# Kernel tuning notes

Hardware: AMD Instinct MI355X
Metric: run time of the kernel (lower is better)

Reference implementation:

```python
import jax, jax.numpy as jnp
import numpy as np

N = 50000   # nodes
E = 800000  # directed edges (self-loops added inside reference)
F_IN, H, C = 128, 96, 32


def setup_inputs() -> dict:
    key = jax.random.key(0)
    ks = jax.random.split(key, 8)
    x = jax.random.normal(ks[0], (N, F_IN), dtype=jnp.float32)
    edge_index = jax.random.randint(ks[1], (2, E), 0, N, dtype=jnp.int64)
    W1 = jax.random.normal(ks[2], (F_IN, H), dtype=jnp.float32) * 0.05
    b1 = jnp.zeros((H,), dtype=jnp.float32)
    W2 = jax.random.normal(ks[3], (H, H), dtype=jnp.float32) * 0.05
    b2 = jnp.zeros((H,), dtype=jnp.float32)
    W3 = jax.random.normal(ks[4], (H, C), dtype=jnp.float32) * 0.05
    b3 = jnp.zeros((C,), dtype=jnp.float32)
    return {"x": x, "edge_index": edge_index, "W1": W1, "b1": b1,
            "W2": W2, "b2": b2, "W3": W3, "b3": b3}


def gcn_conv(x, W, b, src, dst, n):
    """PyG GCNConv: x' = D^{-1/2} (A+I) D^{-1/2} (x W) + b (self-loops in src/dst)."""
    xw = x @ W                                        # [n, out]
    ones = jnp.ones(src.shape[0], dtype=xw.dtype)
    deg = jax.ops.segment_sum(ones, dst, num_segments=n)
    dinv = jnp.where(deg > 0, jax.lax.rsqrt(jnp.maximum(deg, 1.0)), 0.0)
    norm = dinv[src] * dinv[dst]                      # [E+n]
    msg = norm[:, None] * xw[src]                     # gather + scale
    out = jax.ops.segment_sum(msg, dst, num_segments=n)  # scatter-add
    return out + b


def reference(x, edge_index, W1, b1, W2, b2, W3, b3):
    loop = jnp.arange(N, dtype=edge_index.dtype)
    src = jnp.concatenate([edge_index[0], loop])      # add self-loops once
    dst = jnp.concatenate([edge_index[1], loop])
    h = jax.nn.relu(gcn_conv(x, W1, b1, src, dst, N))   # dropout is identity (eval)
    h = jax.nn.relu(gcn_conv(h, W2, b2, src, dst, N))
    h = gcn_conv(h, W3, b3, src, dst, N)
    return jax.nn.log_softmax(h, axis=1)
```

## Files before the change

### kernel.cpp

```cpp
#include <hip/hip_runtime.h>
#include <hip/hip_fp16.h>


typedef _Float16 half8 __attribute__((ext_vector_type(8)));
typedef float f32x4 __attribute__((ext_vector_type(4)));

constexpr int CAP = 64;
constexpr int NPB = 128;
constexpr int NBINS_P = 512;
constexpr int EPB = 4096;
constexpr int BCAP = 2560;

__device__ inline unsigned char f_to_fp8(float f) {
    f = fminf(fmaxf(f, -448.0f), 448.0f);
    unsigned short u = __half_as_ushort(__float2half(f * 0.00390625f));
    unsigned short mag = (unsigned short)((u & 0x7FFF) + 0x40);
    return (unsigned char)(((u >> 8) & 0x80) | (mag >> 7));
}

__device__ inline float2 fp8x2_to_f2_scaled(unsigned int w) {
    unsigned int lo = ((w << 7) & 0x3F80u) | ((w << 8) & 0x8000u);
    unsigned int hi = ((w >> 1) & 0x3F80u) | (w & 0x8000u);
    union { unsigned int u; __half2 h; } cv;
    cv.u = lo | (hi << 16);
    return __half22float2(cv.h);
}

__device__ inline float4 fp8x4_to_f4_scaled(unsigned int w) {
    float2 lo = fp8x2_to_f2_scaled(w & 0xFFFFu);
    float2 hi = fp8x2_to_f2_scaled(w >> 16);
    return {lo.x, lo.y, hi.x, hi.y};
}

__global__ __launch_bounds__(256) void prep_kernel(const int* __restrict__ ei, int twoE,
                                                   int* __restrict__ flags,
                                                   int* __restrict__ bin_cnt,
                                                   const float* __restrict__ W1,
                                                   const float* __restrict__ W2,
                                                   const float* __restrict__ W3,
                                                   __half* __restrict__ Wt1,
                                                   __half* __restrict__ Wt2,
                                                   __half* __restrict__ Wt3) {
    if (blockIdx.x == 0) {
        if (threadIdx.x < 8) flags[threadIdx.x] = 0;
        for (int b = threadIdx.x; b < NBINS_P; b += 256) bin_cnt[b] = 0;
        __syncthreads();
        int c = 0;
        for (int j = threadIdx.x; j < 2048 && j < twoE; j += 256) {
            if ((j & 1) && ei[j] != 0) c++;
        }
        if (c) atomicAdd(&flags[4], c);
        return;
    }
    int i = (blockIdx.x - 1) * 256 + threadIdx.x;
    if (i < 128 * 96) {
        int f = i / 128, k = i - f * 128;
        Wt1[i] = __float2half(W1[(size_t)k * 96 + f]);
    } else if (i < 128 * 96 + 96 * 96) {
        int j = i - 128 * 96;
        int f = j / 96, k = j - f * 96;
        Wt2[j] = __float2half(W2[(size_t)k * 96 + f]);
    } else if (i < 128 * 96 + 96 * 96 + 96 * 32) {
        int j = i - 128 * 96 - 96 * 96;
        int f = j / 96, k = j - f * 96;
        Wt3[j] = __float2half(W3[(size_t)k * 32 + f]);
    }
}

__device__ inline int ld_idx(const int* ei, int half_, int i, int E, bool i64) {
    return i64 ? ei[2 * (half_ * (size_t)E + i)] : ei[half_ * (size_t)E + i];
}

__global__ __launch_bounds__(256) void part_kernel(const int* __restrict__ ei,
                                                   const int* __restrict__ flags,
                                                   int* __restrict__ bin_cnt,
                                                   int* __restrict__ bins, int E, int n) {
    __shared__ int hist[NBINS_P], excl[NBINS_P], cur[NBINS_P], gpos[NBINS_P];
    __shared__ int tmp[256];
    __shared__ int stage[EPB];
    const int tid = threadIdx.x;
    const bool i64 = (flags[4] == 0);
    for (int b = tid; b < NBINS_P; b += 256) hist[b] = 0;
    __syncthreads();

    int v[EPB / 256];
    const int base = blockIdx.x * EPB;
#pragma unroll
    for (int j = 0; j < EPB / 256; j++) {
        int i = base + j * 256 + tid;
        v[j] = -1;
        if (i < E) {
            int s = ld_idx(ei, 0, i, E, i64);
            int d = ld_idx(ei, 1, i, E, i64);
            if ((unsigned)s < (unsigned)n && (unsigned)d < (unsigned)n) {
                int bin = d >> 7, ln = d & 127;
                v[j] = (bin << 23) | (ln << 16) | s;
                atomicAdd(&hist[bin], 1);
            }
        }
    }
    __syncthreads();
    int a0 = hist[2 * tid], a1 = hist[2 * tid + 1];
    int pairsum = a0 + a1;
    tmp[tid] = pairsum;
    __syncthreads();
    for (int off = 1; off < 256; off <<= 1) {
        int t = (tid >= off) ? tmp[tid - off] : 0;
        __syncthreads();
        tmp[tid] += t;
        __syncthreads();
    }
    int S = tmp[tid] - pairsum;
    excl[2 * tid] = S;
    excl[2 * tid + 1] = S + a0;
    cur[2 * tid] = S;
    cur[2 * tid + 1] = S + a0;
    __syncthreads();
    for (int b = tid; b < NBINS_P; b += 256)
        gpos[b] = hist[b] ? atomicAdd(&bin_cnt[b], hist[b]) : 0;
#pragma unroll
    for (int j = 0; j < EPB / 256; j++) {
        if (v[j] != -1) {
            int bin = ((unsigned)v[j]) >> 23;
            int p = atomicAdd(&cur[bin], 1);
            stage[p] = v[j];
        }
    }
    __syncthreads();
    int total = excl[NBINS_P - 1] + hist[NBINS_P - 1];
    for (int i = tid; i < total; i += 256) {
        int w = stage[i];
        int bin = ((unsigned)w) >> 23;
        int k = gpos[bin] + (i - excl[bin]);
        if (k < BCAP) bins[(size_t)bin * BCAP + k] = w;
    }
}

__global__ __launch_bounds__(256) void build_kernel(const int* __restrict__ bin_cnt,
                                                    const int* __restrict__ bins,
                                                    int* __restrict__ cnt,
                                                    unsigned short* __restrict__ csr, int n) {
    __shared__ unsigned short lcsr[NPB * CAP];
    __shared__ int lcnt[NPB];
    const int b = blockIdx.x, tid = threadIdx.x;
    for (int i = tid; i < NPB; i += 256) lcnt[i] = 0;
    __syncthreads();
    int m = min(bin_cnt[b], BCAP);
    for (int i = tid; i < m; i += 256) {
        int w = bins[(size_t)b * BCAP + i];
        int ln = (w >> 16) & 127;
        int p = atomicAdd(&lcnt[ln], 1);
        if (p < CAP) lcsr[ln * CAP + p] = (unsigned short)(w & 0xFFFF);
    }
    __syncthreads();
    const int node0 = b * NPB;
    const unsigned int* l32 = (const unsigned int*)lcsr;
    unsigned int* c32 = (unsigned int*)(csr + (size_t)node0 * CAP);
    for (int i = tid; i < NPB * CAP / 2; i += 256) {
        int node = node0 + (i >> 5);
        if (node < n) c32[i] = l32[i];
    }
    for (int t = tid; t < NPB; t += 256)
        if (node0 + t < n) cnt[node0 + t] = lcnt[t];
}

__device__ inline half8 to_h8(float4 u0, float4 u1) {
    half8 r;
    r[0] = (_Float16)u0.x; r[1] = (_Float16)u0.y; r[2] = (_Float16)u0.z; r[3] = (_Float16)u0.w;
    r[4] = (_Float16)u1.x; r[5] = (_Float16)u1.y; r[6] = (_Float16)u1.z; r[7] = (_Float16)u1.w;
    return r;
}

template <int K, int F, bool XF32, bool OUT8>
__global__ __launch_bounds__(256) void gemm_mfma(const void* __restrict__ X,
                                                 const __half* __restrict__ Wt,
                                                 const int* __restrict__ cnt,
                                                 void* __restrict__ out, int n) {
    constexpr int KP = K + 8;
    constexpr int FT = F / 16;
    constexpr int KC = K / 32;
    __shared__ _Float16 Wl[F * KP];
    for (int i = threadIdx.x; i < F * (K / 8); i += 256) {
        int f = i / (K / 8), c = i - f * (K / 8);
        *(half8*)&Wl[f * KP + c * 8] = *(const half8*)&Wt[(size_t)f * K + c * 8];
    }
    __syncthreads();
    const int wave = threadIdx.x >> 6, lane = threadIdx.x & 63;
    const int node0 = (blockIdx.x * 4 + wave) * 16;
    if (node0 >= n) return;
    const int m = lane & 15, q = lane >> 4;
    const int arow = min(node0 + m, n - 1);

    half8 af[KC];
    if (XF32) {
        const float* xp = (const float*)X + (size_t)arow * K + q * 8;
#pragma unroll
        for (int kc = 0; kc < KC; kc++) {
            float4 u0 = *(const float4*)(xp + kc * 32);
            float4 u1 = *(const float4*)(xp + kc * 32 + 4);
            af[kc] = to_h8(u0, u1);
        }
    } else {
        const __half* xp = (const __half*)X + (size_t)arow * K + q * 8;
#pragma unroll
        for (int kc = 0; kc < KC; kc++) af[kc] = *(const half8*)(xp + kc * 32);
    }

    f32x4 acc[FT];
#pragma unroll
    for (int t = 0; t < FT; t++) acc[t] = (f32x4)0.f;
#pragma unroll
    for (int kc = 0; kc < KC; kc++) {
#pragma unroll
        for (int t = 0; t < FT; t++) {
            half8 b = *(const half8*)&Wl[(t * 16 + m) * KP + kc * 32 + q * 8];
            acc[t] = __builtin_amdgcn_mfma_f32_16x16x32_f16(af[kc], b, acc[t], 0, 0, 0);
        }
    }
    float dv[4];
#pragma unroll
    for (int r = 0; r < 4; r++) {
        int node = node0 + q * 4 + r;
        dv[r] = (node < n) ? rsqrtf(1.0f + (float)cnt[node]) : 0.f;
    }
#pragma unroll
    for (int t = 0; t < FT; t++)
#pragma unroll
        for (int r = 0; r < 4; r++) {
            int node = node0 + q * 4 + r;
            if (node < n) {
                float vv = acc[t][r] * dv[r];
                if (OUT8)
                    ((unsigned char*)out)[(size_t)node * F + t * 16 + m] = f_to_fp8(vv);
                else
                    ((__half*)out)[(size_t)node * F + t * 16 + m] = __float2half(vv);
            }
        }
}

__global__ __launch_bounds__(256) void agg96_fp8(const unsigned char* __restrict__ xws,
                                                 const int* __restrict__ cnt,
                                                 const unsigned short* __restrict__ csr,
                                                 const float* __restrict__ bias,
                                                 __half* __restrict__ out, int n) {
    int node = blockIdx.x * 4 + (threadIdx.x >> 6);
    int lane = threadIdx.x & 63;
    if (node >= n) return;
    const int g = lane < 24 ? 0 : 1;
    const int c = g ? lane - 24 : lane;
    const bool act = lane < 48;
    int deg = cnt[node];
    int m = min(deg, CAP);
    float dvs = rsqrtf(1.0f + (float)deg) * 256.0f;
    const uint4* r4 = (const uint4*)(csr + (size_t)node * CAP);
    float4 a = {0.f, 0.f, 0.f, 0.f};
    if (lane < 24) {
        unsigned int w = *(const unsigned int*)(xws + (size_t)node * 96 + c * 4);
        a = fp8x4_to_f4_scaled(w);
    }
    int e = 0;
#define G96_U(pr_) (g ? ((pr_) >> 16) : ((pr_) & 0xFFFF))
#define G96_LD(u_) (*(const unsigned int*)(xws + (size_t)(u_) * 96 + c * 4))
    for (; e + 16 <= m; e += 16) {
        uint4 pa = r4[e >> 3], pb = r4[(e >> 3) + 1];
        if (act) {
            unsigned int w0 = G96_LD(G96_U(pa.x)), w1 = G96_LD(G96_U(pa.y));
            unsigned int w2 = G96_LD(G96_U(pa.z)), w3 = G96_LD(G96_U(pa.w));
            unsigned int w4 = G96_LD(G96_U(pb.x)), w5 = G96_LD(G96_U(pb.y));
            unsigned int w6 = G96_LD(G96_U(pb.z)), w7 = G96_LD(G96_U(pb.w));
            float4 f;
            f = fp8x4_to_f4_scaled(w0); a.x += f.x; a.y += f.y; a.z += f.z; a.w += f.w;
            f = fp8x4_to_f4_scaled(w1); a.x += f.x; a.y += f.y; a.z += f.z; a.w += f.w;
            f = fp8x4_to_f4_scaled(w2); a.x += f.x; a.y += f.y; a.z += f.z; a.w += f.w;
            f = fp8x4_to_f4_scaled(w3); a.x += f.x; a.y += f.y; a.z += f.z; a.w += f.w;
            f = fp8x4_to_f4_scaled(w4); a.x += f.x; a.y += f.y; a.z += f.z; a.w += f.w;
            f = fp8x4_to_f4_scaled(w5); a.x += f.x; a.y += f.y; a.z += f.z; a.w += f.w;
            f = fp8x4_to_f4_scaled(w6); a.x += f.x; a.y += f.y; a.z += f.z; a.w += f.w;
            f = fp8x4_to_f4_scaled(w7); a.x += f.x; a.y += f.y; a.z += f.z; a.w += f.w;
        }
    }
    if (e + 8 <= m) {
        uint4 pa = r4[e >> 3];
        if (act) {
            unsigned int w0 = G96_LD(G96_U(pa.x)), w1 = G96_LD(G96_U(pa.y));
            unsigned int w2 = G96_LD(G96_U(pa.z)), w3 = G96_LD(G96_U(pa.w));
            float4 f;
            f = fp8x4_to_f4_scaled(w0); a.x += f.x; a.y += f.y; a.z += f.z; a.w += f.w;
            f = fp8x4_to_f4_scaled(w1); a.x += f.x; a.y += f.y; a.z += f.z; a.w += f.w;
            f = fp8x4_to_f4_scaled(w2); a.x += f.x; a.y += f.y; a.z += f.z; a.w += f.w;
            f = fp8x4_to_f4_scaled(w3); a.x += f.x; a.y += f.y; a.z += f.z; a.w += f.w;
        }
        e += 8;
    }
    if (e + 4 <= m) {
        const unsigned int* r2 = (const unsigned int*)r4;
        unsigned int p0 = r2[e >> 1], p1 = r2[(e >> 1) + 1];
        if (act) {
            unsigned int w0 = G96_LD(G96_U(p0)), w1 = G96_LD(G96_U(p1));
            float4 f;
            f = fp8x4_to_f4_scaled(w0); a.x += f.x; a.y += f.y; a.z += f.z; a.w += f.w;
            f = fp8x4_to_f4_scaled(w1); a.x += f.x; a.y += f.y; a.z += f.z; a.w += f.w;
        }
        e += 4;
    }
    if (e + 2 <= m) {
        unsigned int p0 = ((const unsigned int*)r4)[e >> 1];
        if (act) {
            unsigned int w0 = G96_LD(G96_U(p0));
            float4 f = fp8x4_to_f4_scaled(w0);
            a.x += f.x; a.y += f.y; a.z += f.z; a.w += f.w;
        }
        e += 2;
    }
    if (e < m && lane < 24) {
        int u = ((const unsigned short*)r4)[e];
        float4 f = fp8x4_to_f4_scaled(G96_LD(u));
        a.x += f.x; a.y += f.y; a.z += f.z; a.w += f.w;
    }
#undef G96_U
#undef G96_LD
    float px = __shfl(a.x, lane + 24);
    float py = __shfl(a.y, lane + 24);
    float pz = __shfl(a.z, lane + 24);
    float pw = __shfl(a.w, lane + 24);
    if (lane < 24) {
        a.x += px; a.y += py; a.z += pz; a.w += pw;
        float4 bb = *(const float4*)&bias[c * 4];
        float r0 = fmaxf(fmaf(dvs, a.x, bb.x), 0.f);
        float r1 = fmaxf(fmaf(dvs, a.y, bb.y), 0.f);
        float r2 = fmaxf(fmaf(dvs, a.z, bb.z), 0.f);
        float r3 = fmaxf(fmaf(dvs, a.w, bb.w), 0.f);
        union { __half2 h[2]; uint2 u; } pk;
        pk.h[0] = __floats2half2_rn(r0, r1);
        pk.h[1] = __floats2half2_rn(r2, r3);
        *(uint2*)(out + (size_t)node * 96 + c * 4) = pk.u;
    }
}

__global__ __launch_bounds__(256) void agg32_lsm(const __half* __restrict__ xws,
                                                 const int* __restrict__ cnt,
                                                 const unsigned short* __restrict__ csr,
                                                 const float* __restrict__ bias,
                                                 float* __restrict__ out, int n) {
    int node = blockIdx.x * 4 + (threadIdx.x >> 6);
    int lane = threadIdx.x & 63;
    if (node >= n) return;
    const int g = lane >> 4, l = lane & 15;
    int deg = cnt[node];
    int m = min(deg, CAP);
    float dv = rsqrtf(1.0f + (float)deg);
    const uint4* r4 = (const uint4*)(csr + (size_t)node * CAP);
    float2 a = {0.f, 0.f};
    if (g == 0) a = __half22float2(*(const __half2*)(xws + (size_t)node * 32 + l * 2));
    auto ext = [](uint4 p, int j) -> int {
        unsigned int h = (j & 4) ? ((j & 2) ? p.w : p.z) : ((j & 2) ? p.y : p.x);
        return (j & 1) ? (int)(h >> 16) : (int)(h & 0xFFFF);
    };
    int e = 0;
    for (; e + 16 <= m; e += 16) {
        uint4 pa = r4[e >> 3], pb = r4[(e >> 3) + 1];
        int u0 = ext(pa, g), u1 = ext(pa, g + 4);
        int u2 = ext(pb, g), u3 = ext(pb, g + 4);
        float2 f0 = __half22float2(*(const __half2*)(xws + (size_t)u0 * 32 + l * 2));
        float2 f1 = __half22float2(*(const __half2*)(xws + (size_t)u1 * 32 + l * 2));
        float2 f2 = __half22float2(*(const __half2*)(xws + (size_t)u2 * 32 + l * 2));
        float2 f3 = __half22float2(*(const __half2*)(xws + (size_t)u3 * 32 + l * 2));
        a.x += f0.x + f1.x + f2.x + f3.x;
        a.y += f0.y + f1.y + f2.y + f3.y;
    }
    if (e + 8 <= m) {
        uint4 pa = r4[e >> 3];
        int u0 = ext(pa, g), u1 = ext(pa, g + 4);
        float2 f0 = __half22float2(*(const __half2*)(xws + (size_t)u0 * 32 + l * 2));
        float2 f1 = __half22float2(*(const __half2*)(xws + (size_t)u1 * 32 + l * 2));
        a.x += f0.x + f1.x;
        a.y += f0.y + f1.y;
        e += 8;
    }
    if (e + 4 <= m) {
        unsigned int p0 = ((const unsigned int*)r4)[e >> 1];
        unsigned int p1 = ((const unsigned int*)r4)[(e >> 1) + 1];
        unsigned int h = (g & 2) ? p1 : p0;
        int u = (g & 1) ? (int)(h >> 16) : (int)(h & 0xFFFF);
        float2 f = __half22float2(*(const __half2*)(xws + (size_t)u * 32 + l * 2));
        a.x += f.x; a.y += f.y;
        e += 4;
    }
    for (; e < m; e++) {
        if (g == 0) {
            int u = ((const unsigned short*)r4)[e];
            float2 f = __half22float2(*(const __half2*)(xws + (size_t)u * 32 + l * 2));
            a.x += f.x; a.y += f.y;
        }
    }
    a.x += __shfl_xor(a.x, 16); a.y += __shfl_xor(a.y, 16);
    a.x += __shfl_xor(a.x, 32); a.y += __shfl_xor(a.y, 32);
    if (g == 0) {
        float2 b = *(const float2*)&bias[l * 2];
        float rx = fmaf(dv, a.x, b.x), ry = fmaf(dv, a.y, b.y);
        float mx = fmaxf(rx, ry);
        mx = fmaxf(mx, __shfl_xor(mx, 1));
        mx = fmaxf(mx, __shfl_xor(mx, 2));
        mx = fmaxf(mx, __shfl_xor(mx, 4));
        mx = fmaxf(mx, __shfl_xor(mx, 8));
        float s = expf(rx - mx) + expf(ry - mx);
        s += __shfl_xor(s, 1);
        s += __shfl_xor(s, 2);
        s += __shfl_xor(s, 4);
        s += __shfl_xor(s, 8);
        float ls = logf(s);
        ((float2*)out)[(size_t)node * 16 + l] = {rx - mx - ls, ry - mx - ls};
    }
}

extern "C" void kernel_launch(void* const* d_in, const int* in_sizes, int n_in,
                              void* d_out, int out_size, void* d_ws, size_t ws_size,
                              hipStream_t stream) {
    const float* x  = (const float*)d_in[0];
    const int*   ei = (const int*)d_in[1];
    const float* W1 = (const float*)d_in[2];
    const float* b1 = (const float*)d_in[3];
    const float* W2 = (const float*)d_in[4];
    const float* b2 = (const float*)d_in[5];
    const float* W3 = (const float*)d_in[6];
    const float* b3 = (const float*)d_in[7];
    float* out = (float*)d_out;

    const int N_ = in_sizes[0] / 128;
    const int E_ = in_sizes[1] / 2;
    const int NBINS = (N_ + NPB - 1) / NPB;

    char* base = (char*)d_ws;
    size_t off = 0;
    auto take = [&](size_t bytes) {
        void* p = base + off;
        off = (off + bytes + 255) & ~(size_t)255;
        return p;
    };
    int*    flags   = (int*)take(4 * 8);
    int*    bin_cnt = (int*)take(4 * NBINS_P);
    int*    bins    = (int*)take(4 * (size_t)NBINS * BCAP);
    int*    cnt     = (int*)take(4 * (size_t)N_);
    unsigned short* csr = (unsigned short*)take(2 * (size_t)N_ * CAP);
    __half* Wt1     = (__half*)take(2 * 128 * 96);
    __half* Wt2     = (__half*)take(2 * 96 * 96);
    __half* Wt3     = (__half*)take(2 * 96 * 32);
    unsigned char* bufA = (unsigned char*)take(2 * (size_t)N_ * 96);
    __half* bufB    = (__half*)take(2 * (size_t)N_ * 96);

    const int prepBlocks = 1 + (128 * 96 + 96 * 96 + 96 * 32 + 255) / 256;
    prep_kernel<<<prepBlocks, 256, 0, stream>>>(ei, in_sizes[1], flags, bin_cnt,
                                                W1, W2, W3, Wt1, Wt2, Wt3);
    part_kernel<<<(E_ + EPB - 1) / EPB, 256, 0, stream>>>(ei, flags, bin_cnt, bins, E_, N_);
    build_kernel<<<NBINS, 256, 0, stream>>>(bin_cnt, bins, cnt, csr, N_);

    const int gGemm = (N_ + 63) / 64;
    const int gAgg  = (N_ + 3) / 4;

    gemm_mfma<128, 96, true, true><<<gGemm, 256, 0, stream>>>(x, Wt1, cnt, bufA, N_);
    agg96_fp8<<<gAgg, 256, 0, stream>>>(bufA, cnt, csr, b1, bufB, N_);
    gemm_mfma<96, 96, false, true><<<gGemm, 256, 0, stream>>>(bufB, Wt2, cnt, bufA, N_);
    agg96_fp8<<<gAgg, 256, 0, stream>>>(bufA, cnt, csr, b2, bufB, N_);
    gemm_mfma<96, 32, false, false><<<gGemm, 256, 0, stream>>>(bufB, Wt3, cnt, bufA, N_);
    agg32_lsm<<<gAgg, 256, 0, stream>>>((const __half*)bufA, cnt, csr, b3, out, N_);
}
```

Measured before the change: 225.9 us.

## Fold prep into partition kernel and widen agg96 gather to 8-byte lanes

The separate prep kernel goes away. Weight transposition moves into the partition kernel's blocks, each block detects int64 indices itself, and a memset clears the bin counters. This removes one launch and its serial dependency. The 96-wide fp8 aggregation is rewritten so each lane loads 8 bytes and four 12-lane groups process four edges per step, with a two-stage shuffle reduction and 16-byte output stores. Every block now repeats the index-type detection, and the gather loop issues loads for inactive lanes on the node's own row.

```diff
diff --git a/kernel.cpp b/kernel.cpp
--- a/kernel.cpp
+++ b/kernel.cpp
@@ -32,59 +32,56 @@
     return {lo.x, lo.y, hi.x, hi.y};
 }
 
-__global__ __launch_bounds__(256) void prep_kernel(const int* __restrict__ ei, int twoE,
-                                                   int* __restrict__ flags,
+__device__ inline int ld_idx(const int* ei, int half_, int i, int E, bool i64) {
+    return i64 ? ei[2 * (half_ * (size_t)E + i)] : ei[half_ * (size_t)E + i];
+}
+
+__global__ __launch_bounds__(256) void part_kernel(const int* __restrict__ ei,
                                                    int* __restrict__ bin_cnt,
+                                                   int* __restrict__ bins,
                                                    const float* __restrict__ W1,
                                                    const float* __restrict__ W2,
                                                    const float* __restrict__ W3,
                                                    __half* __restrict__ Wt1,
                                                    __half* __restrict__ Wt2,
-                                                   __half* __restrict__ Wt3) {
-    if (blockIdx.x == 0) {
-        if (threadIdx.x < 8) flags[threadIdx.x] = 0;
-        for (int b = threadIdx.x; b < NBINS_P; b += 256) bin_cnt[b] = 0;
-        __syncthreads();
-        int c = 0;
-        for (int j = threadIdx.x; j < 2048 && j < twoE; j += 256) {
-            if ((j & 1) && ei[j] != 0) c++;
-        }
-        if (c) atomicAdd(&flags[4], c);
-        return;
-    }
-    int i = (blockIdx.x - 1) * 256 + threadIdx.x;
-    if (i < 128 * 96) {
-        int f = i / 128, k = i - f * 128;
-        Wt1[i] = __float2half(W1[(size_t)k * 96 + f]);
-    } else if (i < 128 * 96 + 96 * 96) {
-        int j = i - 128 * 96;
-        int f = j / 96, k = j - f * 96;
-        Wt2[j] = __float2half(W2[(size_t)k * 96 + f]);
-    } else if (i < 128 * 96 + 96 * 96 + 96 * 32) {
-        int j = i - 128 * 96 - 96 * 96;
-        int f = j / 96, k = j - f * 96;
-        Wt3[j] = __float2half(W3[(size_t)k * 32 + f]);
-    }
-}
-
-__device__ inline int ld_idx(const int* ei, int half_, int i, int E, bool i64) {
-    return i64 ? ei[2 * (half_ * (size_t)E + i)] : ei[half_ * (size_t)E + i];
-}
-
-__global__ __launch_bounds__(256) void part_kernel(const int* __restrict__ ei,
-                                                   const int* __restrict__ flags,
-                                                   int* __restrict__ bin_cnt,
-                                                   int* __restrict__ bins, int E, int n) {
+                                                   __half* __restrict__ Wt3,
+                                                   int E, int n) {
     __shared__ int hist[NBINS_P], excl[NBINS_P], cur[NBINS_P], gpos[NBINS_P];
     __shared__ int tmp[256];
     __shared__ int stage[EPB];
+    __shared__ int i64flag;
     const int tid = threadIdx.x;
-    const bool i64 = (flags[4] == 0);
+    const int bid = blockIdx.x;
+
+    {
+        int i = bid * 256 + tid;
+        if (i < 128 * 96) {
+            int f = i / 128, k = i - f * 128;
+            Wt1[i] = __float2half(W1[(size_t)k * 96 + f]);
+        } else if (i < 128 * 96 + 96 * 96) {
+            int j = i - 128 * 96;
+            int f = j / 96, k = j - f * 96;
+            Wt2[j] = __float2half(W2[(size_t)k * 96 + f]);
+        } else if (i < 128 * 96 + 96 * 96 + 96 * 32) {
+            int j = i - 128 * 96 - 96 * 96;
+            int f = j / 96, k = j - f * 96;
+            Wt3[j] = __float2half(W3[(size_t)k * 32 + f]);
+        }
+    }
+    if (tid == 0) i64flag = 0;
     for (int b = tid; b < NBINS_P; b += 256) hist[b] = 0;
     __syncthreads();
+    {
+        int cdet = 0, twoE = 2 * E;
+        for (int j = 2 * tid + 1; j < 2048 && j < twoE; j += 512)
+            if (ei[j] != 0) cdet = 1;
+        if (cdet) atomicAdd(&i64flag, 1);
+    }
+    __syncthreads();
+    const bool i64 = (i64flag == 0);
 
     int v[EPB / 256];
-    const int base = blockIdx.x * EPB;
+    const int base = bid * EPB;
 #pragma unroll
     for (int j = 0; j < EPB / 256; j++) {
         int i = base + j * 256 + tid;
@@ -246,94 +243,90 @@
     int node = blockIdx.x * 4 + (threadIdx.x >> 6);
     int lane = threadIdx.x & 63;
     if (node >= n) return;
-    const int g = lane < 24 ? 0 : 1;
-    const int c = g ? lane - 24 : lane;
+    const int g = lane / 12;
+    const int c = lane - g * 12;
     const bool act = lane < 48;
     int deg = cnt[node];
     int m = min(deg, CAP);
     float dvs = rsqrtf(1.0f + (float)deg) * 256.0f;
-    const uint4* r4 = (const uint4*)(csr + (size_t)node * CAP);
-    float4 a = {0.f, 0.f, 0.f, 0.f};
-    if (lane < 24) {
-        unsigned int w = *(const unsigned int*)(xws + (size_t)node * 96 + c * 4);
-        a = fp8x4_to_f4_scaled(w);
-    }
-    int e = 0;
-#define G96_U(pr_) (g ? ((pr_) >> 16) : ((pr_) & 0xFFFF))
-#define G96_LD(u_) (*(const unsigned int*)(xws + (size_t)(u_) * 96 + c * 4))
-    for (; e + 16 <= m; e += 16) {
-        uint4 pa = r4[e >> 3], pb = r4[(e >> 3) + 1];
-        if (act) {
-            unsigned int w0 = G96_LD(G96_U(pa.x)), w1 = G96_LD(G96_U(pa.y));
-            unsigned int w2 = G96_LD(G96_U(pa.z)), w3 = G96_LD(G96_U(pa.w));
-            unsigned int w4 = G96_LD(G96_U(pb.x)), w5 = G96_LD(G96_U(pb.y));
-            unsigned int w6 = G96_LD(G96_U(pb.z)), w7 = G96_LD(G96_U(pb.w));
-            float4 f;
-            f = fp8x4_to_f4_scaled(w0); a.x += f.x; a.y += f.y; a.z += f.z; a.w += f.w;
-            f = fp8x4_to_f4_scaled(w1); a.x += f.x; a.y += f.y; a.z += f.z; a.w += f.w;
-            f = fp8x4_to_f4_scaled(w2); a.x += f.x; a.y += f.y; a.z += f.z; a.w += f.w;
-            f = fp8x4_to_f4_scaled(w3); a.x += f.x; a.y += f.y; a.z += f.z; a.w += f.w;
-            f = fp8x4_to_f4_scaled(w4); a.x += f.x; a.y += f.y; a.z += f.z; a.w += f.w;
-            f = fp8x4_to_f4_scaled(w5); a.x += f.x; a.y += f.y; a.z += f.z; a.w += f.w;
-            f = fp8x4_to_f4_scaled(w6); a.x += f.x; a.y += f.y; a.z += f.z; a.w += f.w;
-            f = fp8x4_to_f4_scaled(w7); a.x += f.x; a.y += f.y; a.z += f.z; a.w += f.w;
-        }
-    }
-    if (e + 8 <= m) {
-        uint4 pa = r4[e >> 3];
-        if (act) {
-            unsigned int w0 = G96_LD(G96_U(pa.x)), w1 = G96_LD(G96_U(pa.y));
-            unsigned int w2 = G96_LD(G96_U(pa.z)), w3 = G96_LD(G96_U(pa.w));
-            float4 f;
-            f = fp8x4_to_f4_scaled(w0); a.x += f.x; a.y += f.y; a.z += f.z; a.w += f.w;
-            f = fp8x4_to_f4_scaled(w1); a.x += f.x; a.y += f.y; a.z += f.z; a.w += f.w;
-            f = fp8x4_to_f4_scaled(w2); a.x += f.x; a.y += f.y; a.z += f.z; a.w += f.w;
-            f = fp8x4_to_f4_scaled(w3); a.x += f.x; a.y += f.y; a.z += f.z; a.w += f.w;
-        }
-        e += 8;
-    }
-    if (e + 4 <= m) {
-        const unsigned int* r2 = (const unsigned int*)r4;
-        unsigned int p0 = r2[e >> 1], p1 = r2[(e >> 1) + 1];
-        if (act) {
-            unsigned int w0 = G96_LD(G96_U(p0)), w1 = G96_LD(G96_U(p1));
-            float4 f;
-            f = fp8x4_to_f4_scaled(w0); a.x += f.x; a.y += f.y; a.z += f.z; a.w += f.w;
-            f = fp8x4_to_f4_scaled(w1); a.x += f.x; a.y += f.y; a.z += f.z; a.w += f.w;
-        }
-        e += 4;
-    }
-    if (e + 2 <= m) {
-        unsigned int p0 = ((const unsigned int*)r4)[e >> 1];
-        if (act) {
-            unsigned int w0 = G96_LD(G96_U(p0));
-            float4 f = fp8x4_to_f4_scaled(w0);
-            a.x += f.x; a.y += f.y; a.z += f.z; a.w += f.w;
-        }
-        e += 2;
-    }
-    if (e < m && lane < 24) {
-        int u = ((const unsigned short*)r4)[e];
-        float4 f = fp8x4_to_f4_scaled(G96_LD(u));
-        a.x += f.x; a.y += f.y; a.z += f.z; a.w += f.w;
-    }
-#undef G96_U
-#undef G96_LD
-    float px = __shfl(a.x, lane + 24);
-    float py = __shfl(a.y, lane + 24);
-    float pz = __shfl(a.z, lane + 24);
-    float pw = __shfl(a.w, lane + 24);
-    if (lane < 24) {
-        a.x += px; a.y += py; a.z += pz; a.w += pw;
-        float4 bb = *(const float4*)&bias[c * 4];
-        float r0 = fmaxf(fmaf(dvs, a.x, bb.x), 0.f);
-        float r1 = fmaxf(fmaf(dvs, a.y, bb.y), 0.f);
-        float r2 = fmaxf(fmaf(dvs, a.z, bb.z), 0.f);
-        float r3 = fmaxf(fmaf(dvs, a.w, bb.w), 0.f);
-        union { __half2 h[2]; uint2 u; } pk;
+    const unsigned int* r2 = (const unsigned int*)(csr + (size_t)node * CAP);
+    float4 A0 = {0.f, 0.f, 0.f, 0.f}, A1 = {0.f, 0.f, 0.f, 0.f};
+    if (g == 0) {
+        uint2 w = *(const uint2*)(xws + (size_t)node * 96 + c * 8);
+        A0 = fp8x4_to_f4_scaled(w.x);
+        A1 = fp8x4_to_f4_scaled(w.y);
+    }
+#define G96_EXT(p_) ((g & 1) ? ((((g & 2) ? 0 : 1) ? (p_) : (p_)) >> 16) : ((p_) & 0xFFFF))
+    auto extu = [&](unsigned int pl, unsigned int ph) -> int {
+        unsigned int h = (g & 2) ? ph : pl;
+        return (g & 1) ? (int)(h >> 16) : (int)(h & 0xFFFF);
+    };
+    auto acc8 = [&](uint2 w) {
+        float4 f0 = fp8x4_to_f4_scaled(w.x);
+        float4 f1 = fp8x4_to_f4_scaled(w.y);
+        A0.x += f0.x; A0.y += f0.y; A0.z += f0.z; A0.w += f0.w;
+        A1.x += f1.x; A1.y += f1.y; A1.z += f1.z; A1.w += f1.w;
+    };
+    int t = 0;
+    const int steps = (m + 3) >> 2;
+    for (; (t + 4) * 4 <= m; t += 4) {
+        unsigned int p0 = r2[2 * t],     p1 = r2[2 * t + 1];
+        unsigned int p2 = r2[2 * t + 2], p3 = r2[2 * t + 3];
+        unsigned int p4 = r2[2 * t + 4], p5 = r2[2 * t + 5];
+        unsigned int p6 = r2[2 * t + 6], p7 = r2[2 * t + 7];
+        int u0 = act ? extu(p0, p1) : node;
+        int u1 = act ? extu(p2, p3) : node;
+        int u2 = act ? extu(p4, p5) : node;
+        int u3 = act ? extu(p6, p7) : node;
+        uint2 w0 = *(const uint2*)(xws + (size_t)u0 * 96 + c * 8);
+        uint2 w1 = *(const uint2*)(xws + (size_t)u1 * 96 + c * 8);
+        uint2 w2 = *(const uint2*)(xws + (size_t)u2 * 96 + c * 8);
+        uint2 w3 = *(const uint2*)(xws + (size_t)u3 * 96 + c * 8);
+        if (act) { acc8(w0); acc8(w1); acc8(w2); acc8(w3); }
+    }
+    for (; t < steps; t++) {
+        unsigned int pl = r2[2 * t], ph = r2[2 * t + 1];
+        bool valid = act && (4 * t + g) < m;
+        int u = valid ? extu(pl, ph) : node;
+        uint2 w = *(const uint2*)(xws + (size_t)u * 96 + c * 8);
+        if (valid) acc8(w);
+    }
+#undef G96_EXT
+    {
+        int s1 = (lane + 24) & 63;
+        float v0 = __shfl(A0.x, s1), v1 = __shfl(A0.y, s1), v2 = __shfl(A0.z, s1),
+              v3 = __shfl(A0.w, s1), v4 = __shfl(A1.x, s1), v5 = __shfl(A1.y, s1),
+              v6 = __shfl(A1.z, s1), v7 = __shfl(A1.w, s1);
+        if (lane < 24) {
+            A0.x += v0; A0.y += v1; A0.z += v2; A0.w += v3;
+            A1.x += v4; A1.y += v5; A1.z += v6; A1.w += v7;
+        }
+        int s2 = (lane + 12) & 63;
+        v0 = __shfl(A0.x, s2); v1 = __shfl(A0.y, s2); v2 = __shfl(A0.z, s2);
+        v3 = __shfl(A0.w, s2); v4 = __shfl(A1.x, s2); v5 = __shfl(A1.y, s2);
+        v6 = __shfl(A1.z, s2); v7 = __shfl(A1.w, s2);
+        if (lane < 12) {
+            A0.x += v0; A0.y += v1; A0.z += v2; A0.w += v3;
+            A1.x += v4; A1.y += v5; A1.z += v6; A1.w += v7;
+        }
+    }
+    if (lane < 12) {
+        float4 b0 = *(const float4*)&bias[c * 8];
+        float4 b1 = *(const float4*)&bias[c * 8 + 4];
+        float r0 = fmaxf(fmaf(dvs, A0.x, b0.x), 0.f);
+        float r1 = fmaxf(fmaf(dvs, A0.y, b0.y), 0.f);
+        float r2_ = fmaxf(fmaf(dvs, A0.z, b0.z), 0.f);
+        float r3 = fmaxf(fmaf(dvs, A0.w, b0.w), 0.f);
+        float r4 = fmaxf(fmaf(dvs, A1.x, b1.x), 0.f);
+        float r5 = fmaxf(fmaf(dvs, A1.y, b1.y), 0.f);
+        float r6 = fmaxf(fmaf(dvs, A1.z, b1.z), 0.f);
+        float r7 = fmaxf(fmaf(dvs, A1.w, b1.w), 0.f);
+        union { __half2 h[4]; uint4 u4; } pk;
         pk.h[0] = __floats2half2_rn(r0, r1);
-        pk.h[1] = __floats2half2_rn(r2, r3);
-        *(uint2*)(out + (size_t)node * 96 + c * 4) = pk.u;
+        pk.h[1] = __floats2half2_rn(r2_, r3);
+        pk.h[2] = __floats2half2_rn(r4, r5);
+        pk.h[3] = __floats2half2_rn(r6, r7);
+        *(uint4*)(out + (size_t)node * 96 + c * 8) = pk.u4;
     }
 }
 
@@ -437,7 +430,6 @@
         off = (off + bytes + 255) & ~(size_t)255;
         return p;
     };
-    int*    flags   = (int*)take(4 * 8);
     int*    bin_cnt = (int*)take(4 * NBINS_P);
     int*    bins    = (int*)take(4 * (size_t)NBINS * BCAP);
     int*    cnt     = (int*)take(4 * (size_t)N_);
@@ -448,10 +440,10 @@
     unsigned char* bufA = (unsigned char*)take(2 * (size_t)N_ * 96);
     __half* bufB    = (__half*)take(2 * (size_t)N_ * 96);
 
-    const int prepBlocks = 1 + (128 * 96 + 96 * 96 + 96 * 32 + 255) / 256;
-    prep_kernel<<<prepBlocks, 256, 0, stream>>>(ei, in_sizes[1], flags, bin_cnt,
-                                                W1, W2, W3, Wt1, Wt2, Wt3);
-    part_kernel<<<(E_ + EPB - 1) / EPB, 256, 0, stream>>>(ei, flags, bin_cnt, bins, E_, N_);
+    hipMemsetAsync(bin_cnt, 0, 4 * NBINS_P, stream);
+    part_kernel<<<(E_ + EPB - 1) / EPB, 256, 0, stream>>>(ei, bin_cnt, bins,
+                                                          W1, W2, W3, Wt1, Wt2, Wt3,
+                                                          E_, N_);
     build_kernel<<<NBINS, 256, 0, stream>>>(bin_cnt, bins, cnt, csr, N_);
 
     const int gGemm = (N_ + 63) / 64;
```

New measurement: 237.4 us. 5.1% more time.
